# Kernel optimization log

Hardware: AMD Instinct MI355X
Metric: run time of the kernel (lower is better)

## Reference

```python
import jax, jax.numpy as jnp
import numpy as np

BLOCK_SIZE = 32
BLOCK_COUNTS = 16
B, N, H, D = 4, 1024, 8, 64
LENGTHS = np.array([1024, 768, 512, 896], dtype=np.int64)


def setup_inputs() -> dict:
    key = jax.random.key(0)
    ks = jax.random.split(key, 8)
    offsets = np.concatenate([[0], np.cumsum(LENGTHS)]).astype(np.int32)
    mask = np.zeros((B, N), dtype=bool)
    for b in range(B):
        mask[b, : int(LENGTHS[b])] = True
    gather_idx = np.nonzero(mask.reshape(-1))[0].astype(np.int32)
    m = jnp.asarray(mask)[:, :, None, None].astype(jnp.float32)
    padded_q = jax.random.normal(ks[0], (B, N, H, D), jnp.float32) * m
    padded_k = jax.random.normal(ks[1], (B, N, H, D), jnp.float32) * m
    padded_v = jax.random.normal(ks[2], (B, N, H, D), jnp.float32) * m
    gidx = jnp.asarray(gather_idx)
    jagged_q = padded_q.reshape(B * N, H, D)[gidx]
    jagged_k = padded_k.reshape(B * N, H, D)[gidx]
    jagged_v = padded_v.reshape(B * N, H, D)[gidx]
    jagged_u = jax.random.normal(ks[3], (int(gidx.shape[0]), H, D), jnp.float32)
    gate_w = jax.random.normal(ks[4], (H, D, 3), jnp.float32) * 0.1
    return {"jagged_q": jagged_q, "jagged_k": jagged_k, "jagged_v": jagged_v,
            "jagged_u": jagged_u, "padded_q": padded_q, "padded_k": padded_k,
            "padded_v": padded_v, "x_offsets": jnp.asarray(offsets),
            "gate_w": gate_w, "padding_mask": jnp.asarray(mask),
            "gather_idx": gidx}


def _forward(jagged_q, jagged_k, jagged_v, padded_q, padded_k, padded_v,
             x_offsets, gate_w, gather_idx):
    scale = D ** -0.5
    nb = N // BLOCK_SIZE                                   # N is a multiple of BLOCK_SIZE (pad_len=0)
    S = min(BLOCK_COUNTS, nb)
    lengths = x_offsets[1:] - x_offsets[:-1]               # [B]
    cmp_len = (lengths + BLOCK_SIZE - 1) // BLOCK_SIZE     # [B] valid compressed blocks per seq
    pos = jnp.arange(N)
    blk = jnp.arange(nb)
    q_blk = pos // BLOCK_SIZE

    # scatter jagged tokens back to dense padded layout (zeros at padding) --
    # the Triton kernels read q/k/v from the jagged tensors.
    def to_dense(j):
        return jnp.zeros((B * N, H, D), j.dtype).at[gather_idx].set(j).reshape(B, N, H, D)
    qd, kd, vd = to_dense(jagged_q), to_dense(jagged_k), to_dense(jagged_v)

    # gates: per-token/per-head sigmoid linear gate from padded_q -> (g_cmp, g_slc, g_swa)
    gates = jax.nn.sigmoid(jnp.einsum('bnhd,hdg->bnhg', padded_q, gate_w))
    g_cmp, g_slc = gates[..., 0], gates[..., 1]            # g_swa unused by this module

    # compressed (block-mean) keys / values  [B, nb, H, D]
    k_cmp = padded_k.reshape(B, nb, BLOCK_SIZE, H, D).mean(axis=2)
    v_cmp = padded_v.reshape(B, nb, BLOCK_SIZE, H, D).mean(axis=2)

    # ---- compressed branch: SiLU attention over block-mean keys ----
    s_cmp = jnp.einsum('bqhd,bkhd->bqhk', qd, k_cmp) * scale          # [B,N,H,nb]
    mask_cmp = (q_blk[:, None] >= blk[None, :])[None, :, None, :] & \
               (blk[None, None, None, :] < cmp_len[:, None, None, None])
    p_cmp = jnp.where(mask_cmp, jax.nn.silu(s_cmp), 0.0)
    o_cmp = jnp.einsum('bqhk,bkhd->bqhd', p_cmp, v_cmp) * g_cmp[..., None]

    # ---- block selection: causal top-k over compressed scores ----
    s_sel = jnp.einsum('bqhd,bkhd->bhqk', padded_q, k_cmp) * scale    # [B,H,N,nb]
    causal_blk = (q_blk[:, None] >= blk[None, :])[None, None]
    _, top_idx = jax.lax.top_k(jnp.where(causal_blk, s_sel, -jnp.inf), S)  # [B,H,N,S]
    top_idx = jnp.where(top_idx > q_blk[None, None, :, None], -1, top_idx)
    top_idx = top_idx.transpose(0, 2, 1, 3)                           # [B,N,H,S]

    # ---- selected branch: SiLU attention restricted to selected blocks ----
    blk_sel = jnp.any(top_idx[..., None] == blk, axis=-2)             # [B,N,H,nb] (-1 matches nothing)
    key_sel = jnp.repeat(blk_sel, BLOCK_SIZE, axis=-1)                # [B,N,H,N]
    mask_slc = key_sel & (pos[:, None] >= pos[None, :])[None, :, None, :]
    s_slc = jnp.einsum('bqhd,bkhd->bqhk', qd, kd) * scale             # [B,N,H,N]
    p_slc = jnp.where(mask_slc, jax.nn.silu(s_slc), 0.0)
    o_slc = jnp.einsum('bqhk,bkhd->bqhd', p_slc, vd) * g_slc[..., None]

    # jagged output: gather valid tokens
    return (o_cmp + o_slc).reshape(B * N, H, D)[gather_idx]


def reference(jagged_q, jagged_k, jagged_v, jagged_u, padded_q, padded_k,
              padded_v, x_offsets, gate_w, padding_mask, gather_idx):
    return _forward(jagged_q, jagged_k, jagged_v, padded_q, padded_k,
                    padded_v, x_offsets, gate_w, gather_idx)
```

## Files before the change

### kernel.cpp

```cpp
#include <hip/hip_runtime.h>
#include <math.h>
#include <stdint.h>

#define BB 4
#define NN 1024
#define HH 8
#define DD 64
#define BS 32
#define NB 32
#define SS 16

typedef __attribute__((ext_vector_type(8)))  short bf16x8;
typedef __attribute__((ext_vector_type(16))) float f32x16;
typedef __attribute__((ext_vector_type(2)))  int   int2v;

union FragU { bf16x8 h; uint32_t u[4]; };

#define ZERO16 {0.f,0.f,0.f,0.f,0.f,0.f,0.f,0.f,0.f,0.f,0.f,0.f,0.f,0.f,0.f,0.f}

__device__ __forceinline__ uint32_t cvt_pk_bf16(float lo, float hi) {
    uint32_t r;
    asm("v_cvt_pk_bf16_f32 %0, %1, %2" : "=v"(r) : "v"(lo), "v"(hi));
    return r;
}

__device__ __forceinline__ uint16_t bf16_rne(float x) {
    uint32_t fb = __float_as_uint(x);
    return (uint16_t)((fb + 0x7fffu + ((fb >> 16) & 1u)) >> 16);
}

__device__ __forceinline__ float silu_f(float x) {
    return __fdividef(x, 1.f + __expf(-x));
}

__global__ __launch_bounds__(256) void prep_kernel(
    const float* __restrict__ pk, const float* __restrict__ pv,
    uint16_t* __restrict__ Kb, uint16_t* __restrict__ Vt,
    float* __restrict__ kc, uint16_t* __restrict__ vct)
{
    __shared__ float klds[32][65];
    __shared__ float vlds[32][65];
    const int t = threadIdx.x;
    const int blk = blockIdx.x & 31;
    const int h = (blockIdx.x >> 5) & 7;
    const int b = blockIdx.x >> 8;
    const int bh = b * 8 + h;

    const int r = t >> 3;
    const int dg = (t & 7) * 8;
    size_t sbase = (((size_t)(b * NN + blk * BS + r)) * HH + h) * DD + dg;
    float4 ka = *(const float4*)(pk + sbase);
    float4 kb4 = *(const float4*)(pk + sbase + 4);
    float4 va = *(const float4*)(pv + sbase);
    float4 vb4 = *(const float4*)(pv + sbase + 4);

    FragU kf;
    kf.u[0] = cvt_pk_bf16(ka.x, ka.y);  kf.u[1] = cvt_pk_bf16(ka.z, ka.w);
    kf.u[2] = cvt_pk_bf16(kb4.x, kb4.y); kf.u[3] = cvt_pk_bf16(kb4.z, kb4.w);
    *(bf16x8*)(Kb + (((size_t)bh * NN) + blk * BS + r) * DD + dg) = kf.h;

    *(float4*)&klds[r][dg] = ka;  *(float4*)&klds[r][dg + 4] = kb4;
    *(float4*)&vlds[r][dg] = va;  *(float4*)&vlds[r][dg + 4] = vb4;
    __syncthreads();

    if (t < 64) {
        float s = 0.f;
        #pragma unroll
        for (int j = 0; j < 32; ++j) s += klds[j][t];
        kc[((size_t)bh * NB + blk) * DD + t] = s * (1.f / BS);
    } else if (t < 128) {
        int d = t - 64;
        float s = 0.f;
        #pragma unroll
        for (int j = 0; j < 32; ++j) s += vlds[j][d];
        vct[((size_t)bh * DD + d) * NB + blk] = bf16_rne(s * (1.f / BS));
    }

    {
        int d = t >> 2, ng = (t & 3) * 8;
        float p0 = vlds[ng + 0][d], p1 = vlds[ng + 1][d];
        float p2 = vlds[ng + 2][d], p3 = vlds[ng + 3][d];
        float p4 = vlds[ng + 4][d], p5 = vlds[ng + 5][d];
        float p6 = vlds[ng + 6][d], p7 = vlds[ng + 7][d];
        FragU vf;
        vf.u[0] = cvt_pk_bf16(p0, p1); vf.u[1] = cvt_pk_bf16(p2, p3);
        vf.u[2] = cvt_pk_bf16(p4, p5); vf.u[3] = cvt_pk_bf16(p6, p7);
        *(bf16x8*)(Vt + ((size_t)bh * DD + d) * NN + blk * BS + ng) = vf.h;
    }
}

__global__ __launch_bounds__(256, 4) void bsa_mfma_kernel(
    const float* __restrict__ pq, const uint16_t* __restrict__ Kb,
    const uint16_t* __restrict__ Vt, const float* __restrict__ kc,
    const uint16_t* __restrict__ vct, const float* __restrict__ gw,
    const int* __restrict__ xoff, float* __restrict__ out)
{
    __shared__ float qlds[32][64];
    __shared__ __align__(16) uint16_t pcmp[32][40];
    __shared__ uint32_t selmask[32];
    __shared__ float gateC[32], gateS[32];
    __shared__ float olds[32][64];

    const int tid = threadIdx.x;
    const int lane = tid & 63;
    const int w = tid >> 6;
    const int l31 = lane & 31;
    const int hi = lane >> 5;

    const int bid = blockIdx.x;
    const int h = bid & 7;
    const int rem = bid >> 3;
    const int qb = rem & 31;
    const int b = rem >> 5;
    const int bh = b * 8 + h;

    const int off0 = xoff[b];
    const int len = xoff[b + 1] - off0;
    if (qb * BS >= len) return;

    {
        int q = tid >> 3, d = (tid & 7) * 8;
        *(float4*)&olds[q][d] = make_float4(0.f, 0.f, 0.f, 0.f);
        *(float4*)&olds[q][d + 4] = make_float4(0.f, 0.f, 0.f, 0.f);
    }

    {
        int q = tid >> 3, part = (tid & 7) * 8;
        const float* src = pq + (((size_t)(b * NN + qb * BS + q)) * HH + h) * DD + part;
        *(float4*)&qlds[q][part] = *(const float4*)src;
        *(float4*)&qlds[q][part + 4] = *(const float4*)(src + 4);
    }

    FragU qf[4];
    {
        const float* qrow = pq + (((size_t)(b * NN + qb * BS + l31)) * HH + h) * DD;
        #pragma unroll
        for (int t = 0; t < 4; ++t) {
            const float* qp = qrow + t * 16 + hi * 8;
            float4 x = *(const float4*)qp;
            float4 y = *(const float4*)(qp + 4);
            qf[t].u[0] = cvt_pk_bf16(x.x, x.y);
            qf[t].u[1] = cvt_pk_bf16(x.z, x.w);
            qf[t].u[2] = cvt_pk_bf16(y.x, y.y);
            qf[t].u[3] = cvt_pk_bf16(y.z, y.w);
        }
    }

    float4 kcv[8];
    {
        const float* kcrow = kc + ((size_t)bh * NB + l31) * DD + hi * 32;
        #pragma unroll
        for (int i = 0; i < 8; ++i) kcv[i] = *(const float4*)(kcrow + i * 4);
    }

    __syncthreads();

    for (int j = 0; j < 8; ++j) {
        int q = w * 8 + j;
        const float* qv = qlds[q];
        const float* qh = qv + hi * 32;
        float part = 0.f;
        #pragma unroll
        for (int i = 0; i < 8; ++i) {
            float4 qq = *(const float4*)(qh + i * 4);
            part += qq.x * kcv[i].x + qq.y * kcv[i].y + qq.z * kcv[i].z + qq.w * kcv[i].w;
        }
        float s = (part + __shfl_xor(part, 32)) * 0.125f;
        float p = (l31 <= qb) ? silu_f(s) : 0.f;
        if (lane < 32) pcmp[q][l31] = bf16_rne(p);
        uint32_t m;
        if (qb >= SS) {
            float vsel = (l31 <= qb) ? s : -INFINITY;
            int rank = 0;
            #pragma unroll
            for (int off = 1; off < 32; ++off) {
                float o = __shfl_xor(vsel, off);
                int oi = l31 ^ off;
                rank += (o > vsel || (o == vsel && oi < l31)) ? 1 : 0;
            }
            m = (uint32_t)(__ballot(rank < SS) & 0xffffffffu);
        } else {
            m = (1u << (qb + 1)) - 1u;
        }
        if (lane == 0) selmask[q] = m;
        float qd = qv[lane];
        float g0 = qd * gw[(h * DD + lane) * 3 + 0];
        float g1 = qd * gw[(h * DD + lane) * 3 + 1];
        #pragma unroll
        for (int off = 32; off; off >>= 1) {
            g0 += __shfl_xor(g0, off);
            g1 += __shfl_xor(g1, off);
        }
        if (lane == 0) {
            gateC[q] = __frcp_rn(1.f + __expf(-g0));
            gateS[q] = __frcp_rn(1.f + __expf(-g1));
        }
    }

    __syncthreads();

    const uint32_t mymask = selmask[l31];
    uint32_t tmask = mymask;
    #pragma unroll
    for (int off = 1; off < 32; off <<= 1) tmask |= __shfl_xor(tmask, off);

    if (w == 3) {
        f32x16 c0 = ZERO16, c1 = ZERO16;
        #pragma unroll
        for (int s = 0; s < 2; ++s) {
            FragU pa;
            pa.h = *(const bf16x8*)&pcmp[l31][s * 16 + hi * 8];
            #pragma unroll
            for (int dh = 0; dh < 2; ++dh) {
                FragU vb;
                vb.h = *(const bf16x8*)(vct + ((size_t)bh * DD + dh * 32 + l31) * NB + s * 16 + hi * 8);
                if (dh == 0) c0 = __builtin_amdgcn_mfma_f32_32x32x16_bf16(pa.h, vb.h, c0, 0, 0, 0);
                else         c1 = __builtin_amdgcn_mfma_f32_32x32x16_bf16(pa.h, vb.h, c1, 0, 0, 0);
            }
        }
        #pragma unroll
        for (int r = 0; r < 16; ++r) {
            int q = (r & 3) + 8 * (r >> 2) + 4 * hi;
            float gc = gateC[q];
            atomicAdd(&olds[q][l31], gc * c0[r]);
            atomicAdd(&olds[q][32 + l31], gc * c1[r]);
        }
    }

    f32x16 accO0 = ZERO16, accO1 = ZERO16;
    bool any = false;
    const int qpos = qb * BS + l31;
    {
        uint32_t m = tmask;
        int bcnt = 0;
        while (m) {
            int kb = __builtin_ctz(m); m &= m - 1;
            if (((bcnt++) & 3) != w) continue;
            any = true;
            f32x16 accS = ZERO16;
            const uint16_t* krow = Kb + (((size_t)bh * NN) + kb * BS + l31) * DD;
            #pragma unroll
            for (int t = 0; t < 4; ++t) {
                FragU kf;
                kf.h = *(const bf16x8*)(krow + t * 16 + hi * 8);
                accS = __builtin_amdgcn_mfma_f32_32x32x16_bf16(kf.h, qf[t].h, accS, 0, 0, 0);
            }
            const bool selbit = (mymask >> kb) & 1;
            const bool notdiag = kb < qb;
            float pr[16];
            #pragma unroll
            for (int r = 0; r < 16; ++r) {
                int key = (r & 3) + 8 * (r >> 2) + 4 * hi;
                int kpos = kb * BS + key;
                float s = accS[r] * 0.125f;
                bool ok = selbit && (notdiag || kpos <= qpos);
                pr[r] = ok ? silu_f(s) : 0.f;
            }
            uint32_t wv[8];
            #pragma unroll
            for (int i = 0; i < 8; ++i) wv[i] = cvt_pk_bf16(pr[2 * i], pr[2 * i + 1]);
            int2v e0 = __builtin_amdgcn_permlane32_swap(wv[0], wv[2], false, false);
            int2v e1 = __builtin_amdgcn_permlane32_swap(wv[1], wv[3], false, false);
            int2v e2 = __builtin_amdgcn_permlane32_swap(wv[4], wv[6], false, false);
            int2v e3 = __builtin_amdgcn_permlane32_swap(wv[5], wv[7], false, false);
            FragU a0, a1;
            a0.u[0] = e0[0]; a0.u[1] = e1[0]; a0.u[2] = e0[1]; a0.u[3] = e1[1];
            a1.u[0] = e2[0]; a1.u[1] = e3[0]; a1.u[2] = e2[1]; a1.u[3] = e3[1];
            #pragma unroll
            for (int s = 0; s < 2; ++s) {
                const FragU& pa = s ? a1 : a0;
                #pragma unroll
                for (int dh = 0; dh < 2; ++dh) {
                    FragU vb;
                    vb.h = *(const bf16x8*)(Vt + ((size_t)bh * DD + dh * 32 + l31) * NN + kb * BS + s * 16 + hi * 8);
                    if (dh == 0) accO0 = __builtin_amdgcn_mfma_f32_32x32x16_bf16(pa.h, vb.h, accO0, 0, 0, 0);
                    else         accO1 = __builtin_amdgcn_mfma_f32_32x32x16_bf16(pa.h, vb.h, accO1, 0, 0, 0);
                }
            }
        }
    }

    if (any) {
        #pragma unroll
        for (int r = 0; r < 16; ++r) {
            int q = (r & 3) + 8 * (r >> 2) + 4 * hi;
            float gs = gateS[q];
            atomicAdd(&olds[q][l31], gs * accO0[r]);
            atomicAdd(&olds[q][32 + l31], gs * accO1[r]);
        }
    }

    __syncthreads();

    {
        int q = tid >> 3, dpart = (tid & 7) * 8;
        int pos = qb * BS + q;
        if (pos < len) {
            float* op = out + (((size_t)(off0 + pos)) * HH + h) * DD + dpart;
            *(float4*)op = *(float4*)&olds[q][dpart];
            *(float4*)(op + 4) = *(float4*)&olds[q][dpart + 4];
        }
    }
}

extern "C" void kernel_launch(void* const* d_in, const int* in_sizes, int n_in,
                              void* d_out, int out_size, void* d_ws, size_t ws_size,
                              hipStream_t stream) {
    const float* pq = (const float*)d_in[4];
    const float* pk = (const float*)d_in[5];
    const float* pv = (const float*)d_in[6];
    const int* xoff = (const int*)d_in[7];
    const float* gw = (const float*)d_in[8];
    float* out = (float*)d_out;

    uint16_t* Kb = (uint16_t*)d_ws;
    uint16_t* Vt = Kb + (size_t)BB * HH * NN * DD;
    float* kc = (float*)(Vt + (size_t)BB * HH * NN * DD);
    uint16_t* vct = (uint16_t*)(kc + (size_t)BB * HH * NB * DD);

    prep_kernel<<<BB * HH * NB, 256, 0, stream>>>(pk, pv, Kb, Vt, kc, vct);
    bsa_mfma_kernel<<<BB * HH * NB, 256, 0, stream>>>(pq, Kb, Vt, kc, vct, gw, xoff, out);
}
```

Measured before the change: 173.8 us.

## Use persistent atomic work queue with heavy-first tiles and double-buffered K/V loads

The attention kernel becomes persistent, launched with 768 blocks. Each block repeatedly takes a query-block tile from a per-head atomic counter, which prep_kernel resets. Tiles are handed out in descending query-block order so the longest causal tiles start first, and the selected K/V fragments for the next block are loaded into registers while the current block is computed. The 1/sqrt(D) scale is folded into the bf16 K and the compressed K during prep, and the per-element scale and diagonal check are dropped for off-diagonal blocks. The aim is to fix load imbalance and idle padded blocks and to hide global load latency, at the cost of higher register pressure (launch bounds lowered to 3) and extra barriers per tile.

```diff
diff --git a/kernel.cpp b/kernel.cpp
--- a/kernel.cpp
+++ b/kernel.cpp
@@ -9,12 +9,18 @@
 #define BS 32
 #define NB 32
 #define SS 16
+#define NT 128
 
 typedef __attribute__((ext_vector_type(8)))  short bf16x8;
 typedef __attribute__((ext_vector_type(16))) float f32x16;
 typedef __attribute__((ext_vector_type(2)))  int   int2v;
 
 union FragU { bf16x8 h; uint32_t u[4]; };
+
+struct KVBuf {
+    FragU k0, k1, k2, k3;
+    FragU v00, v10, v01, v11;
+};
 
 #define ZERO16 {0.f,0.f,0.f,0.f,0.f,0.f,0.f,0.f,0.f,0.f,0.f,0.f,0.f,0.f,0.f,0.f}
 
@@ -36,11 +42,13 @@
 __global__ __launch_bounds__(256) void prep_kernel(
     const float* __restrict__ pk, const float* __restrict__ pv,
     uint16_t* __restrict__ Kb, uint16_t* __restrict__ Vt,
-    float* __restrict__ kc, uint16_t* __restrict__ vct)
+    float* __restrict__ kc, uint16_t* __restrict__ vct,
+    int* __restrict__ cnt)
 {
     __shared__ float klds[32][65];
     __shared__ float vlds[32][65];
     const int t = threadIdx.x;
+    if (blockIdx.x == 0 && t < 8) cnt[t] = 0;
     const int blk = blockIdx.x & 31;
     const int h = (blockIdx.x >> 5) & 7;
     const int b = blockIdx.x >> 8;
@@ -55,8 +63,10 @@
     float4 vb4 = *(const float4*)(pv + sbase + 4);
 
     FragU kf;
-    kf.u[0] = cvt_pk_bf16(ka.x, ka.y);  kf.u[1] = cvt_pk_bf16(ka.z, ka.w);
-    kf.u[2] = cvt_pk_bf16(kb4.x, kb4.y); kf.u[3] = cvt_pk_bf16(kb4.z, kb4.w);
+    kf.u[0] = cvt_pk_bf16(ka.x * 0.125f, ka.y * 0.125f);
+    kf.u[1] = cvt_pk_bf16(ka.z * 0.125f, ka.w * 0.125f);
+    kf.u[2] = cvt_pk_bf16(kb4.x * 0.125f, kb4.y * 0.125f);
+    kf.u[3] = cvt_pk_bf16(kb4.z * 0.125f, kb4.w * 0.125f);
     *(bf16x8*)(Kb + (((size_t)bh * NN) + blk * BS + r) * DD + dg) = kf.h;
 
     *(float4*)&klds[r][dg] = ka;  *(float4*)&klds[r][dg + 4] = kb4;
@@ -67,7 +77,7 @@
         float s = 0.f;
         #pragma unroll
         for (int j = 0; j < 32; ++j) s += klds[j][t];
-        kc[((size_t)bh * NB + blk) * DD + t] = s * (1.f / BS);
+        kc[((size_t)bh * NB + blk) * DD + t] = s * (0.125f / BS);
     } else if (t < 128) {
         int d = t - 64;
         float s = 0.f;
@@ -89,216 +99,247 @@
     }
 }
 
-__global__ __launch_bounds__(256, 4) void bsa_mfma_kernel(
+__device__ __forceinline__ void load_kv(KVBuf& bu, const uint16_t* __restrict__ Kb,
+                                        const uint16_t* __restrict__ Vt,
+                                        int bh, int kb, int l31, int hi)
+{
+    const uint16_t* krow = Kb + (((size_t)bh * NN) + kb * BS + l31) * DD + hi * 8;
+    bu.k0.h = *(const bf16x8*)(krow);
+    bu.k1.h = *(const bf16x8*)(krow + 16);
+    bu.k2.h = *(const bf16x8*)(krow + 32);
+    bu.k3.h = *(const bf16x8*)(krow + 48);
+    const uint16_t* vrow = Vt + ((size_t)bh * DD + l31) * NN + kb * BS + hi * 8;
+    bu.v00.h = *(const bf16x8*)(vrow);
+    bu.v10.h = *(const bf16x8*)(vrow + 16);
+    const uint16_t* vrow1 = vrow + 32 * NN;
+    bu.v01.h = *(const bf16x8*)(vrow1);
+    bu.v11.h = *(const bf16x8*)(vrow1 + 16);
+}
+
+__global__ __launch_bounds__(256, 3) void bsa_mfma_kernel(
     const float* __restrict__ pq, const uint16_t* __restrict__ Kb,
     const uint16_t* __restrict__ Vt, const float* __restrict__ kc,
     const uint16_t* __restrict__ vct, const float* __restrict__ gw,
-    const int* __restrict__ xoff, float* __restrict__ out)
+    const int* __restrict__ xoff, int* __restrict__ cnt,
+    float* __restrict__ out)
 {
     __shared__ float qlds[32][64];
     __shared__ __align__(16) uint16_t pcmp[32][40];
     __shared__ uint32_t selmask[32];
     __shared__ float gateC[32], gateS[32];
     __shared__ float olds[32][64];
+    __shared__ int tile_s;
 
     const int tid = threadIdx.x;
     const int lane = tid & 63;
     const int w = tid >> 6;
     const int l31 = lane & 31;
     const int hi = lane >> 5;
-
-    const int bid = blockIdx.x;
-    const int h = bid & 7;
-    const int rem = bid >> 3;
-    const int qb = rem & 31;
-    const int b = rem >> 5;
-    const int bh = b * 8 + h;
-
-    const int off0 = xoff[b];
-    const int len = xoff[b + 1] - off0;
-    if (qb * BS >= len) return;
-
-    {
-        int q = tid >> 3, d = (tid & 7) * 8;
-        *(float4*)&olds[q][d] = make_float4(0.f, 0.f, 0.f, 0.f);
-        *(float4*)&olds[q][d + 4] = make_float4(0.f, 0.f, 0.f, 0.f);
-    }
-
-    {
-        int q = tid >> 3, part = (tid & 7) * 8;
-        const float* src = pq + (((size_t)(b * NN + qb * BS + q)) * HH + h) * DD + part;
-        *(float4*)&qlds[q][part] = *(const float4*)src;
-        *(float4*)&qlds[q][part + 4] = *(const float4*)(src + 4);
-    }
-
-    FragU qf[4];
-    {
-        const float* qrow = pq + (((size_t)(b * NN + qb * BS + l31)) * HH + h) * DD;
+    const int h = blockIdx.x & 7;
+
+    for (;;) {
+        __syncthreads();
+        if (tid == 0) tile_s = atomicAdd(&cnt[h], 1);
+        __syncthreads();
+        const int idx = tile_s;
+        if (idx >= NT) break;
+        const int qb = 31 - (idx >> 2);
+        const int b = idx & 3;
+        const int bh = b * 8 + h;
+
+        const int off0 = xoff[b];
+        const int len = xoff[b + 1] - off0;
+        if (qb * BS >= len) continue;
+
+        {
+            int q = tid >> 3, d = (tid & 7) * 8;
+            *(float4*)&olds[q][d] = make_float4(0.f, 0.f, 0.f, 0.f);
+            *(float4*)&olds[q][d + 4] = make_float4(0.f, 0.f, 0.f, 0.f);
+            const float* src = pq + (((size_t)(b * NN + qb * BS + q)) * HH + h) * DD + d;
+            *(float4*)&qlds[q][d] = *(const float4*)src;
+            *(float4*)&qlds[q][d + 4] = *(const float4*)(src + 4);
+        }
+
+        FragU qf[4];
+        {
+            const float* qrow = pq + (((size_t)(b * NN + qb * BS + l31)) * HH + h) * DD;
+            #pragma unroll
+            for (int t = 0; t < 4; ++t) {
+                const float* qp = qrow + t * 16 + hi * 8;
+                float4 x = *(const float4*)qp;
+                float4 y = *(const float4*)(qp + 4);
+                qf[t].u[0] = cvt_pk_bf16(x.x, x.y);
+                qf[t].u[1] = cvt_pk_bf16(x.z, x.w);
+                qf[t].u[2] = cvt_pk_bf16(y.x, y.y);
+                qf[t].u[3] = cvt_pk_bf16(y.z, y.w);
+            }
+        }
+
+        float4 kcv[8];
+        {
+            const float* kcrow = kc + ((size_t)bh * NB + l31) * DD + hi * 32;
+            #pragma unroll
+            for (int i = 0; i < 8; ++i) kcv[i] = *(const float4*)(kcrow + i * 4);
+        }
+
+        __syncthreads();
+
+        for (int j = 0; j < 8; ++j) {
+            int q = w * 8 + j;
+            const float* qv = qlds[q];
+            const float* qh = qv + hi * 32;
+            float part = 0.f;
+            #pragma unroll
+            for (int i = 0; i < 8; ++i) {
+                float4 qq = *(const float4*)(qh + i * 4);
+                part += qq.x * kcv[i].x + qq.y * kcv[i].y + qq.z * kcv[i].z + qq.w * kcv[i].w;
+            }
+            float s = part + __shfl_xor(part, 32);
+            float p = (l31 <= qb) ? silu_f(s) : 0.f;
+            if (lane < 32) pcmp[q][l31] = bf16_rne(p);
+            uint32_t m;
+            if (qb >= SS) {
+                float vsel = (l31 <= qb) ? s : -INFINITY;
+                int rank = 0;
+                #pragma unroll
+                for (int off = 1; off < 32; ++off) {
+                    float o = __shfl_xor(vsel, off);
+                    int oi = l31 ^ off;
+                    rank += (o > vsel || (o == vsel && oi < l31)) ? 1 : 0;
+                }
+                m = (uint32_t)(__ballot(rank < SS) & 0xffffffffu);
+            } else {
+                m = (1u << (qb + 1)) - 1u;
+            }
+            if (lane == 0) selmask[q] = m;
+            float qd = qv[lane];
+            float g0 = qd * gw[(h * DD + lane) * 3 + 0];
+            float g1 = qd * gw[(h * DD + lane) * 3 + 1];
+            #pragma unroll
+            for (int off = 32; off; off >>= 1) {
+                g0 += __shfl_xor(g0, off);
+                g1 += __shfl_xor(g1, off);
+            }
+            if (lane == 0) {
+                gateC[q] = __frcp_rn(1.f + __expf(-g0));
+                gateS[q] = __frcp_rn(1.f + __expf(-g1));
+            }
+        }
+
+        __syncthreads();
+
+        const uint32_t mymask = selmask[l31];
+        uint32_t tmask = mymask;
         #pragma unroll
-        for (int t = 0; t < 4; ++t) {
-            const float* qp = qrow + t * 16 + hi * 8;
-            float4 x = *(const float4*)qp;
-            float4 y = *(const float4*)(qp + 4);
-            qf[t].u[0] = cvt_pk_bf16(x.x, x.y);
-            qf[t].u[1] = cvt_pk_bf16(x.z, x.w);
-            qf[t].u[2] = cvt_pk_bf16(y.x, y.y);
-            qf[t].u[3] = cvt_pk_bf16(y.z, y.w);
-        }
-    }
-
-    float4 kcv[8];
-    {
-        const float* kcrow = kc + ((size_t)bh * NB + l31) * DD + hi * 32;
-        #pragma unroll
-        for (int i = 0; i < 8; ++i) kcv[i] = *(const float4*)(kcrow + i * 4);
-    }
-
-    __syncthreads();
-
-    for (int j = 0; j < 8; ++j) {
-        int q = w * 8 + j;
-        const float* qv = qlds[q];
-        const float* qh = qv + hi * 32;
-        float part = 0.f;
-        #pragma unroll
-        for (int i = 0; i < 8; ++i) {
-            float4 qq = *(const float4*)(qh + i * 4);
-            part += qq.x * kcv[i].x + qq.y * kcv[i].y + qq.z * kcv[i].z + qq.w * kcv[i].w;
-        }
-        float s = (part + __shfl_xor(part, 32)) * 0.125f;
-        float p = (l31 <= qb) ? silu_f(s) : 0.f;
-        if (lane < 32) pcmp[q][l31] = bf16_rne(p);
-        uint32_t m;
-        if (qb >= SS) {
-            float vsel = (l31 <= qb) ? s : -INFINITY;
-            int rank = 0;
-            #pragma unroll
-            for (int off = 1; off < 32; ++off) {
-                float o = __shfl_xor(vsel, off);
-                int oi = l31 ^ off;
-                rank += (o > vsel || (o == vsel && oi < l31)) ? 1 : 0;
-            }
-            m = (uint32_t)(__ballot(rank < SS) & 0xffffffffu);
-        } else {
-            m = (1u << (qb + 1)) - 1u;
-        }
-        if (lane == 0) selmask[q] = m;
-        float qd = qv[lane];
-        float g0 = qd * gw[(h * DD + lane) * 3 + 0];
-        float g1 = qd * gw[(h * DD + lane) * 3 + 1];
-        #pragma unroll
-        for (int off = 32; off; off >>= 1) {
-            g0 += __shfl_xor(g0, off);
-            g1 += __shfl_xor(g1, off);
-        }
-        if (lane == 0) {
-            gateC[q] = __frcp_rn(1.f + __expf(-g0));
-            gateS[q] = __frcp_rn(1.f + __expf(-g1));
-        }
-    }
-
-    __syncthreads();
-
-    const uint32_t mymask = selmask[l31];
-    uint32_t tmask = mymask;
-    #pragma unroll
-    for (int off = 1; off < 32; off <<= 1) tmask |= __shfl_xor(tmask, off);
-
-    if (w == 3) {
-        f32x16 c0 = ZERO16, c1 = ZERO16;
-        #pragma unroll
-        for (int s = 0; s < 2; ++s) {
-            FragU pa;
-            pa.h = *(const bf16x8*)&pcmp[l31][s * 16 + hi * 8];
-            #pragma unroll
-            for (int dh = 0; dh < 2; ++dh) {
-                FragU vb;
-                vb.h = *(const bf16x8*)(vct + ((size_t)bh * DD + dh * 32 + l31) * NB + s * 16 + hi * 8);
-                if (dh == 0) c0 = __builtin_amdgcn_mfma_f32_32x32x16_bf16(pa.h, vb.h, c0, 0, 0, 0);
-                else         c1 = __builtin_amdgcn_mfma_f32_32x32x16_bf16(pa.h, vb.h, c1, 0, 0, 0);
-            }
-        }
-        #pragma unroll
-        for (int r = 0; r < 16; ++r) {
-            int q = (r & 3) + 8 * (r >> 2) + 4 * hi;
-            float gc = gateC[q];
-            atomicAdd(&olds[q][l31], gc * c0[r]);
-            atomicAdd(&olds[q][32 + l31], gc * c1[r]);
-        }
-    }
-
-    f32x16 accO0 = ZERO16, accO1 = ZERO16;
-    bool any = false;
-    const int qpos = qb * BS + l31;
-    {
-        uint32_t m = tmask;
-        int bcnt = 0;
-        while (m) {
-            int kb = __builtin_ctz(m); m &= m - 1;
-            if (((bcnt++) & 3) != w) continue;
-            any = true;
-            f32x16 accS = ZERO16;
-            const uint16_t* krow = Kb + (((size_t)bh * NN) + kb * BS + l31) * DD;
-            #pragma unroll
-            for (int t = 0; t < 4; ++t) {
-                FragU kf;
-                kf.h = *(const bf16x8*)(krow + t * 16 + hi * 8);
-                accS = __builtin_amdgcn_mfma_f32_32x32x16_bf16(kf.h, qf[t].h, accS, 0, 0, 0);
-            }
-            const bool selbit = (mymask >> kb) & 1;
-            const bool notdiag = kb < qb;
-            float pr[16];
-            #pragma unroll
-            for (int r = 0; r < 16; ++r) {
-                int key = (r & 3) + 8 * (r >> 2) + 4 * hi;
-                int kpos = kb * BS + key;
-                float s = accS[r] * 0.125f;
-                bool ok = selbit && (notdiag || kpos <= qpos);
-                pr[r] = ok ? silu_f(s) : 0.f;
-            }
-            uint32_t wv[8];
-            #pragma unroll
-            for (int i = 0; i < 8; ++i) wv[i] = cvt_pk_bf16(pr[2 * i], pr[2 * i + 1]);
-            int2v e0 = __builtin_amdgcn_permlane32_swap(wv[0], wv[2], false, false);
-            int2v e1 = __builtin_amdgcn_permlane32_swap(wv[1], wv[3], false, false);
-            int2v e2 = __builtin_amdgcn_permlane32_swap(wv[4], wv[6], false, false);
-            int2v e3 = __builtin_amdgcn_permlane32_swap(wv[5], wv[7], false, false);
-            FragU a0, a1;
-            a0.u[0] = e0[0]; a0.u[1] = e1[0]; a0.u[2] = e0[1]; a0.u[3] = e1[1];
-            a1.u[0] = e2[0]; a1.u[1] = e3[0]; a1.u[2] = e2[1]; a1.u[3] = e3[1];
+        for (int off = 1; off < 32; off <<= 1) tmask |= __shfl_xor(tmask, off);
+
+        if (w == 3) {
+            f32x16 c0 = ZERO16, c1 = ZERO16;
             #pragma unroll
             for (int s = 0; s < 2; ++s) {
-                const FragU& pa = s ? a1 : a0;
+                FragU pa;
+                pa.h = *(const bf16x8*)&pcmp[l31][s * 16 + hi * 8];
                 #pragma unroll
                 for (int dh = 0; dh < 2; ++dh) {
                     FragU vb;
-                    vb.h = *(const bf16x8*)(Vt + ((size_t)bh * DD + dh * 32 + l31) * NN + kb * BS + s * 16 + hi * 8);
-                    if (dh == 0) accO0 = __builtin_amdgcn_mfma_f32_32x32x16_bf16(pa.h, vb.h, accO0, 0, 0, 0);
-                    else         accO1 = __builtin_amdgcn_mfma_f32_32x32x16_bf16(pa.h, vb.h, accO1, 0, 0, 0);
+                    vb.h = *(const bf16x8*)(vct + ((size_t)bh * DD + dh * 32 + l31) * NB + s * 16 + hi * 8);
+                    if (dh == 0) c0 = __builtin_amdgcn_mfma_f32_32x32x16_bf16(pa.h, vb.h, c0, 0, 0, 0);
+                    else         c1 = __builtin_amdgcn_mfma_f32_32x32x16_bf16(pa.h, vb.h, c1, 0, 0, 0);
                 }
             }
-        }
-    }
-
-    if (any) {
-        #pragma unroll
-        for (int r = 0; r < 16; ++r) {
-            int q = (r & 3) + 8 * (r >> 2) + 4 * hi;
-            float gs = gateS[q];
-            atomicAdd(&olds[q][l31], gs * accO0[r]);
-            atomicAdd(&olds[q][32 + l31], gs * accO1[r]);
-        }
-    }
-
-    __syncthreads();
-
-    {
-        int q = tid >> 3, dpart = (tid & 7) * 8;
-        int pos = qb * BS + q;
-        if (pos < len) {
-            float* op = out + (((size_t)(off0 + pos)) * HH + h) * DD + dpart;
-            *(float4*)op = *(float4*)&olds[q][dpart];
-            *(float4*)(op + 4) = *(float4*)&olds[q][dpart + 4];
+            #pragma unroll
+            for (int r = 0; r < 16; ++r) {
+                int q = (r & 3) + 8 * (r >> 2) + 4 * hi;
+                float gc = gateC[q];
+                atomicAdd(&olds[q][l31], gc * c0[r]);
+                atomicAdd(&olds[q][32 + l31], gc * c1[r]);
+            }
+        }
+
+        uint32_t mw = 0;
+        {
+            uint32_t m = tmask; int c = 0;
+            while (m) {
+                int kb = __builtin_ctz(m); m &= m - 1;
+                if (((c++) & 3) == w) mw |= (1u << kb);
+            }
+        }
+
+        f32x16 accO0 = ZERO16, accO1 = ZERO16;
+        const bool any = (mw != 0);
+        const int qpos = qb * BS + l31;
+        if (any) {
+            KVBuf bufA, bufB;
+            int kbA = __builtin_ctz(mw);
+            uint32_t rem = mw & (mw - 1);
+            load_kv(bufA, Kb, Vt, bh, kbA, l31, hi);
+            for (;;) {
+                const bool haveB = (rem != 0);
+                int kbB = 0;
+                if (haveB) {
+                    kbB = __builtin_ctz(rem);
+                    rem &= rem - 1;
+                    load_kv(bufB, Kb, Vt, bh, kbB, l31, hi);
+                }
+                f32x16 accS = ZERO16;
+                accS = __builtin_amdgcn_mfma_f32_32x32x16_bf16(bufA.k0.h, qf[0].h, accS, 0, 0, 0);
+                accS = __builtin_amdgcn_mfma_f32_32x32x16_bf16(bufA.k1.h, qf[1].h, accS, 0, 0, 0);
+                accS = __builtin_amdgcn_mfma_f32_32x32x16_bf16(bufA.k2.h, qf[2].h, accS, 0, 0, 0);
+                accS = __builtin_amdgcn_mfma_f32_32x32x16_bf16(bufA.k3.h, qf[3].h, accS, 0, 0, 0);
+                const bool selbit = (mymask >> kbA) & 1;
+                float pr[16];
+                if (kbA == qb) {
+                    #pragma unroll
+                    for (int r = 0; r < 16; ++r) {
+                        int key = (r & 3) + 8 * (r >> 2) + 4 * hi;
+                        int kpos = kbA * BS + key;
+                        bool ok = selbit && (kpos <= qpos);
+                        pr[r] = ok ? silu_f(accS[r]) : 0.f;
+                    }
+                } else {
+                    #pragma unroll
+                    for (int r = 0; r < 16; ++r)
+                        pr[r] = selbit ? silu_f(accS[r]) : 0.f;
+                }
+                uint32_t wv[8];
+                #pragma unroll
+                for (int i = 0; i < 8; ++i) wv[i] = cvt_pk_bf16(pr[2 * i], pr[2 * i + 1]);
+                int2v e0 = __builtin_amdgcn_permlane32_swap(wv[0], wv[2], false, false);
+                int2v e1 = __builtin_amdgcn_permlane32_swap(wv[1], wv[3], false, false);
+                int2v e2 = __builtin_amdgcn_permlane32_swap(wv[4], wv[6], false, false);
+                int2v e3 = __builtin_amdgcn_permlane32_swap(wv[5], wv[7], false, false);
+                FragU a0, a1;
+                a0.u[0] = e0[0]; a0.u[1] = e1[0]; a0.u[2] = e0[1]; a0.u[3] = e1[1];
+                a1.u[0] = e2[0]; a1.u[1] = e3[0]; a1.u[2] = e2[1]; a1.u[3] = e3[1];
+                accO0 = __builtin_amdgcn_mfma_f32_32x32x16_bf16(a0.h, bufA.v00.h, accO0, 0, 0, 0);
+                accO1 = __builtin_amdgcn_mfma_f32_32x32x16_bf16(a0.h, bufA.v01.h, accO1, 0, 0, 0);
+                accO0 = __builtin_amdgcn_mfma_f32_32x32x16_bf16(a1.h, bufA.v10.h, accO0, 0, 0, 0);
+                accO1 = __builtin_amdgcn_mfma_f32_32x32x16_bf16(a1.h, bufA.v11.h, accO1, 0, 0, 0);
+                if (!haveB) break;
+                bufA = bufB; kbA = kbB;
+            }
+        }
+
+        if (any) {
+            #pragma unroll
+            for (int r = 0; r < 16; ++r) {
+                int q = (r & 3) + 8 * (r >> 2) + 4 * hi;
+                float gs = gateS[q];
+                atomicAdd(&olds[q][l31], gs * accO0[r]);
+                atomicAdd(&olds[q][32 + l31], gs * accO1[r]);
+            }
+        }
+
+        __syncthreads();
+
+        {
+            int q = tid >> 3, dpart = (tid & 7) * 8;
+            int pos = qb * BS + q;
+            if (pos < len) {
+                float* op = out + (((size_t)(off0 + pos)) * HH + h) * DD + dpart;
+                *(float4*)op = *(float4*)&olds[q][dpart];
+                *(float4*)(op + 4) = *(float4*)&olds[q][dpart + 4];
+            }
         }
     }
 }
@@ -317,7 +358,8 @@
     uint16_t* Vt = Kb + (size_t)BB * HH * NN * DD;
     float* kc = (float*)(Vt + (size_t)BB * HH * NN * DD);
     uint16_t* vct = (uint16_t*)(kc + (size_t)BB * HH * NB * DD);
-
-    prep_kernel<<<BB * HH * NB, 256, 0, stream>>>(pk, pv, Kb, Vt, kc, vct);
-    bsa_mfma_kernel<<<BB * HH * NB, 256, 0, stream>>>(pq, Kb, Vt, kc, vct, gw, xoff, out);
-}
+    int* cnt = (int*)(vct + (size_t)BB * HH * DD * NB);
+
+    prep_kernel<<<BB * HH * NB, 256, 0, stream>>>(pk, pv, Kb, Vt, kc, vct, cnt);
+    bsa_mfma_kernel<<<768, 256, 0, stream>>>(pq, Kb, Vt, kc, vct, gw, xoff, cnt, out);
+}
```

Measured after the change: 186.5 us. +7.3%, slower.

## Double-buffer K fragments, fold softmax scale into K, reorder blocks heavy-first

Applied to the files above, without the earlier changes.

Folds the 1/sqrt(D) scale into the bf16 K copy and the compressed-key means in the prep kernel, so the attention kernel no longer multiplies scores by the scale. The selected-block loop now prefetches the next block's K fragments into a second register buffer while the current block computes, and loads V early. The block index order is remapped so high query blocks, which carry the most causal work, are scheduled first, and gate weights are hoisted out of the per-query loop. Keeping two K buffers live raises register pressure, which could lower occupancy under the 256x4 launch bound.

```diff
diff --git a/kernel.cpp b/kernel.cpp
--- a/kernel.cpp
+++ b/kernel.cpp
@@ -41,9 +41,10 @@
     __shared__ float klds[32][65];
     __shared__ float vlds[32][65];
     const int t = threadIdx.x;
-    const int blk = blockIdx.x & 31;
-    const int h = (blockIdx.x >> 5) & 7;
-    const int b = blockIdx.x >> 8;
+    const int h = blockIdx.x & 7;
+    const int rest = blockIdx.x >> 3;
+    const int blk = rest & 31;
+    const int b = rest >> 5;
     const int bh = b * 8 + h;
 
     const int r = t >> 3;
@@ -55,8 +56,10 @@
     float4 vb4 = *(const float4*)(pv + sbase + 4);
 
     FragU kf;
-    kf.u[0] = cvt_pk_bf16(ka.x, ka.y);  kf.u[1] = cvt_pk_bf16(ka.z, ka.w);
-    kf.u[2] = cvt_pk_bf16(kb4.x, kb4.y); kf.u[3] = cvt_pk_bf16(kb4.z, kb4.w);
+    kf.u[0] = cvt_pk_bf16(ka.x * 0.125f, ka.y * 0.125f);
+    kf.u[1] = cvt_pk_bf16(ka.z * 0.125f, ka.w * 0.125f);
+    kf.u[2] = cvt_pk_bf16(kb4.x * 0.125f, kb4.y * 0.125f);
+    kf.u[3] = cvt_pk_bf16(kb4.z * 0.125f, kb4.w * 0.125f);
     *(bf16x8*)(Kb + (((size_t)bh * NN) + blk * BS + r) * DD + dg) = kf.h;
 
     *(float4*)&klds[r][dg] = ka;  *(float4*)&klds[r][dg + 4] = kb4;
@@ -67,7 +70,7 @@
         float s = 0.f;
         #pragma unroll
         for (int j = 0; j < 32; ++j) s += klds[j][t];
-        kc[((size_t)bh * NB + blk) * DD + t] = s * (1.f / BS);
+        kc[((size_t)bh * NB + blk) * DD + t] = s * (0.125f / BS);
     } else if (t < 128) {
         int d = t - 64;
         float s = 0.f;
@@ -87,6 +90,16 @@
         vf.u[2] = cvt_pk_bf16(p4, p5); vf.u[3] = cvt_pk_bf16(p6, p7);
         *(bf16x8*)(Vt + ((size_t)bh * DD + d) * NN + blk * BS + ng) = vf.h;
     }
+}
+
+__device__ __forceinline__ void load_k(FragU* K, const uint16_t* __restrict__ Kb,
+                                       int bh, int kb, int l31, int hi)
+{
+    const uint16_t* krow = Kb + (((size_t)bh * NN) + kb * BS + l31) * DD + hi * 8;
+    K[0].h = *(const bf16x8*)(krow);
+    K[1].h = *(const bf16x8*)(krow + 16);
+    K[2].h = *(const bf16x8*)(krow + 32);
+    K[3].h = *(const bf16x8*)(krow + 48);
 }
 
 __global__ __launch_bounds__(256, 4) void bsa_mfma_kernel(
@@ -107,11 +120,10 @@
     const int l31 = lane & 31;
     const int hi = lane >> 5;
 
-    const int bid = blockIdx.x;
-    const int h = bid & 7;
-    const int rem = bid >> 3;
-    const int qb = rem & 31;
-    const int b = rem >> 5;
+    const int h = blockIdx.x & 7;
+    const int j = blockIdx.x >> 3;
+    const int qb = 31 - (j >> 2);
+    const int b = j & 3;
     const int bh = b * 8 + h;
 
     const int off0 = xoff[b];
@@ -122,13 +134,9 @@
         int q = tid >> 3, d = (tid & 7) * 8;
         *(float4*)&olds[q][d] = make_float4(0.f, 0.f, 0.f, 0.f);
         *(float4*)&olds[q][d + 4] = make_float4(0.f, 0.f, 0.f, 0.f);
-    }
-
-    {
-        int q = tid >> 3, part = (tid & 7) * 8;
-        const float* src = pq + (((size_t)(b * NN + qb * BS + q)) * HH + h) * DD + part;
-        *(float4*)&qlds[q][part] = *(const float4*)src;
-        *(float4*)&qlds[q][part + 4] = *(const float4*)(src + 4);
+        const float* src = pq + (((size_t)(b * NN + qb * BS + q)) * HH + h) * DD + d;
+        *(float4*)&qlds[q][d] = *(const float4*)src;
+        *(float4*)&qlds[q][d + 4] = *(const float4*)(src + 4);
     }
 
     FragU qf[4];
@@ -152,11 +160,13 @@
         #pragma unroll
         for (int i = 0; i < 8; ++i) kcv[i] = *(const float4*)(kcrow + i * 4);
     }
+    const float gwc = gw[(h * DD + lane) * 3 + 0];
+    const float gws = gw[(h * DD + lane) * 3 + 1];
 
     __syncthreads();
 
-    for (int j = 0; j < 8; ++j) {
-        int q = w * 8 + j;
+    for (int jq = 0; jq < 8; ++jq) {
+        int q = w * 8 + jq;
         const float* qv = qlds[q];
         const float* qh = qv + hi * 32;
         float part = 0.f;
@@ -165,7 +175,7 @@
             float4 qq = *(const float4*)(qh + i * 4);
             part += qq.x * kcv[i].x + qq.y * kcv[i].y + qq.z * kcv[i].z + qq.w * kcv[i].w;
         }
-        float s = (part + __shfl_xor(part, 32)) * 0.125f;
+        float s = part + __shfl_xor(part, 32);
         float p = (l31 <= qb) ? silu_f(s) : 0.f;
         if (lane < 32) pcmp[q][l31] = bf16_rne(p);
         uint32_t m;
@@ -184,8 +194,8 @@
         }
         if (lane == 0) selmask[q] = m;
         float qd = qv[lane];
-        float g0 = qd * gw[(h * DD + lane) * 3 + 0];
-        float g1 = qd * gw[(h * DD + lane) * 3 + 1];
+        float g0 = qd * gwc;
+        float g1 = qd * gws;
         #pragma unroll
         for (int off = 32; off; off >>= 1) {
             g0 += __shfl_xor(g0, off);
@@ -227,60 +237,78 @@
         }
     }
 
-    f32x16 accO0 = ZERO16, accO1 = ZERO16;
-    bool any = false;
-    const int qpos = qb * BS + l31;
-    {
-        uint32_t m = tmask;
-        int bcnt = 0;
+    uint32_t mw = 0;
+    {
+        uint32_t m = tmask; int c = 0;
         while (m) {
             int kb = __builtin_ctz(m); m &= m - 1;
-            if (((bcnt++) & 3) != w) continue;
-            any = true;
-            f32x16 accS = ZERO16;
-            const uint16_t* krow = Kb + (((size_t)bh * NN) + kb * BS + l31) * DD;
-            #pragma unroll
-            for (int t = 0; t < 4; ++t) {
-                FragU kf;
-                kf.h = *(const bf16x8*)(krow + t * 16 + hi * 8);
-                accS = __builtin_amdgcn_mfma_f32_32x32x16_bf16(kf.h, qf[t].h, accS, 0, 0, 0);
-            }
-            const bool selbit = (mymask >> kb) & 1;
-            const bool notdiag = kb < qb;
-            float pr[16];
-            #pragma unroll
-            for (int r = 0; r < 16; ++r) {
-                int key = (r & 3) + 8 * (r >> 2) + 4 * hi;
-                int kpos = kb * BS + key;
-                float s = accS[r] * 0.125f;
-                bool ok = selbit && (notdiag || kpos <= qpos);
-                pr[r] = ok ? silu_f(s) : 0.f;
-            }
-            uint32_t wv[8];
-            #pragma unroll
-            for (int i = 0; i < 8; ++i) wv[i] = cvt_pk_bf16(pr[2 * i], pr[2 * i + 1]);
-            int2v e0 = __builtin_amdgcn_permlane32_swap(wv[0], wv[2], false, false);
-            int2v e1 = __builtin_amdgcn_permlane32_swap(wv[1], wv[3], false, false);
-            int2v e2 = __builtin_amdgcn_permlane32_swap(wv[4], wv[6], false, false);
-            int2v e3 = __builtin_amdgcn_permlane32_swap(wv[5], wv[7], false, false);
-            FragU a0, a1;
-            a0.u[0] = e0[0]; a0.u[1] = e1[0]; a0.u[2] = e0[1]; a0.u[3] = e1[1];
-            a1.u[0] = e2[0]; a1.u[1] = e3[0]; a1.u[2] = e2[1]; a1.u[3] = e3[1];
-            #pragma unroll
-            for (int s = 0; s < 2; ++s) {
-                const FragU& pa = s ? a1 : a0;
-                #pragma unroll
-                for (int dh = 0; dh < 2; ++dh) {
-                    FragU vb;
-                    vb.h = *(const bf16x8*)(Vt + ((size_t)bh * DD + dh * 32 + l31) * NN + kb * BS + s * 16 + hi * 8);
-                    if (dh == 0) accO0 = __builtin_amdgcn_mfma_f32_32x32x16_bf16(pa.h, vb.h, accO0, 0, 0, 0);
-                    else         accO1 = __builtin_amdgcn_mfma_f32_32x32x16_bf16(pa.h, vb.h, accO1, 0, 0, 0);
-                }
-            }
-        }
+            if (((c++) & 3) == w) mw |= (1u << kb);
+        }
+    }
+
+    f32x16 accO0 = ZERO16, accO1 = ZERO16;
+    const bool any = (mw != 0);
+    const int qpos = qb * BS + l31;
+
+    #define COMPUTE_BLOCK(KBUF, KBIDX)                                          \
+    {                                                                           \
+        const int kbc = (KBIDX);                                                \
+        f32x16 accS = ZERO16;                                                   \
+        accS = __builtin_amdgcn_mfma_f32_32x32x16_bf16(KBUF[0].h, qf[0].h, accS, 0, 0, 0); \
+        accS = __builtin_amdgcn_mfma_f32_32x32x16_bf16(KBUF[1].h, qf[1].h, accS, 0, 0, 0); \
+        accS = __builtin_amdgcn_mfma_f32_32x32x16_bf16(KBUF[2].h, qf[2].h, accS, 0, 0, 0); \
+        accS = __builtin_amdgcn_mfma_f32_32x32x16_bf16(KBUF[3].h, qf[3].h, accS, 0, 0, 0); \
+        const uint16_t* vrow = Vt + ((size_t)bh * DD + l31) * NN + kbc * BS + hi * 8; \
+        FragU v00, v10, v01, v11;                                               \
+        v00.h = *(const bf16x8*)(vrow);                                         \
+        v10.h = *(const bf16x8*)(vrow + 16);                                    \
+        v01.h = *(const bf16x8*)(vrow + 32 * NN);                               \
+        v11.h = *(const bf16x8*)(vrow + 32 * NN + 16);                          \
+        const bool selbit = (mymask >> kbc) & 1;                                \
+        float pr[16];                                                           \
+        if (kbc == qb) {                                                        \
+            _Pragma("unroll")                                                   \
+            for (int r = 0; r < 16; ++r) {                                      \
+                int key = (r & 3) + 8 * (r >> 2) + 4 * hi;                      \
+                bool ok = selbit && (kbc * BS + key <= qpos);                   \
+                pr[r] = ok ? silu_f(accS[r]) : 0.f;                             \
+            }                                                                   \
+        } else {                                                                \
+            _Pragma("unroll")                                                   \
+            for (int r = 0; r < 16; ++r)                                        \
+                pr[r] = selbit ? silu_f(accS[r]) : 0.f;                         \
+        }                                                                       \
+        uint32_t wv[8];                                                         \
+        _Pragma("unroll")                                                       \
+        for (int i = 0; i < 8; ++i) wv[i] = cvt_pk_bf16(pr[2 * i], pr[2 * i + 1]); \
+        int2v e0 = __builtin_amdgcn_permlane32_swap(wv[0], wv[2], false, false); \
+        int2v e1 = __builtin_amdgcn_permlane32_swap(wv[1], wv[3], false, false); \
+        int2v e2 = __builtin_amdgcn_permlane32_swap(wv[4], wv[6], false, false); \
+        int2v e3 = __builtin_amdgcn_permlane32_swap(wv[5], wv[7], false, false); \
+        FragU a0, a1;                                                           \
+        a0.u[0] = e0[0]; a0.u[1] = e1[0]; a0.u[2] = e0[1]; a0.u[3] = e1[1];     \
+        a1.u[0] = e2[0]; a1.u[1] = e3[0]; a1.u[2] = e2[1]; a1.u[3] = e3[1];     \
+        accO0 = __builtin_amdgcn_mfma_f32_32x32x16_bf16(a0.h, v00.h, accO0, 0, 0, 0); \
+        accO1 = __builtin_amdgcn_mfma_f32_32x32x16_bf16(a0.h, v01.h, accO1, 0, 0, 0); \
+        accO0 = __builtin_amdgcn_mfma_f32_32x32x16_bf16(a1.h, v10.h, accO0, 0, 0, 0); \
+        accO1 = __builtin_amdgcn_mfma_f32_32x32x16_bf16(a1.h, v11.h, accO1, 0, 0, 0); \
     }
 
     if (any) {
+        FragU KA[4], KB[4];
+        int kbA = __builtin_ctz(mw);
+        uint32_t rem = mw & (mw - 1);
+        load_k(KA, Kb, bh, kbA, l31, hi);
+        for (;;) {
+            bool hasB = (rem != 0); int kbB = 0;
+            if (hasB) { kbB = __builtin_ctz(rem); rem &= rem - 1; load_k(KB, Kb, bh, kbB, l31, hi); }
+            COMPUTE_BLOCK(KA, kbA);
+            if (!hasB) break;
+            bool hasA = (rem != 0);
+            if (hasA) { kbA = __builtin_ctz(rem); rem &= rem - 1; load_k(KA, Kb, bh, kbA, l31, hi); }
+            COMPUTE_BLOCK(KB, kbB);
+            if (!hasA) break;
+        }
         #pragma unroll
         for (int r = 0; r < 16; ++r) {
             int q = (r & 3) + 8 * (r >> 2) + 4 * hi;
@@ -289,6 +317,7 @@
             atomicAdd(&olds[q][32 + l31], gs * accO1[r]);
         }
     }
+    #undef COMPUTE_BLOCK
 
     __syncthreads();
 
```

New measurement: 182.4 us. 4.9% more time.
